# Kernel optimization log

Hardware: AMD Instinct MI355X
Metric: run time of the kernel (lower is better)

The kernel has to match this reference:

```python
import math
import jax, jax.numpy as jnp
import numpy as np

B, T, D = 2048, 50, 256
NEG = -100000.0

def setup_inputs() -> dict:
    key = jax.random.key(0)
    ks = jax.random.split(key, 9)
    return {
        "x": jax.random.normal(ks[0], (B, T, D), dtype=jnp.float32),
        "mask": jax.random.randint(ks[1], (B, T, 1), 0, 2, dtype=jnp.int32),
        "time_decay": jax.random.uniform(ks[2], (B, T, 1), dtype=jnp.float32),
        "Wq": jax.random.normal(ks[3], (D, D), dtype=jnp.float32) * (1.0 / math.sqrt(D)),
        "bq": jax.random.normal(ks[4], (D,), dtype=jnp.float32) * 0.01,
        "Wk": jax.random.normal(ks[5], (D, D), dtype=jnp.float32) * (1.0 / math.sqrt(D)),
        "bk": jax.random.normal(ks[6], (D,), dtype=jnp.float32) * 0.01,
        "Wv": jax.random.normal(ks[7], (D, D), dtype=jnp.float32) * (1.0 / math.sqrt(D)),
        "bv": jax.random.normal(ks[8], (D,), dtype=jnp.float32) * 0.01,
    }

def reference(x, mask, time_decay, Wq, bq, Wk, bk, Wv, bv):
    # PositionalEncoding.forward: elementwise multiply by time-decay (broadcast over d_model)
    x = x * time_decay  # [B,T,D]
    q = jnp.einsum('btd,ed->bte', x, Wq) + bq
    k = jnp.einsum('btd,ed->bte', x, Wk) + bk
    v = jnp.einsum('btd,ed->bte', x, Wv) + bv
    # unusual Q/K-side masking (masked_fill before the matmul)
    keep = mask != 0  # [B,T,1]
    q = jnp.where(keep, q, NEG)
    k = jnp.where(keep, k, NEG)
    score = jnp.einsum('btd,bsd->bts', q, k) / math.sqrt(D)  # [B,T,T]
    score = jax.nn.softmax(score, axis=-1)
    # dropout is identity in eval mode
    out = jnp.einsum('bts,bsd->btd', score, v)  # [B,T,D]
    return out[:, -1, :]  # [B,D]
```

## Files before the change

### kernel.cpp

```cpp
#include <hip/hip_runtime.h>


namespace {
constexpr int kB = 2048;
constexpr int kT = 50;
constexpr int kD = 256;
constexpr int kG = 4;
constexpr int kThr = 256;
constexpr double kNeg = -100000.0;
}

__global__ __launch_bounds__(kThr) void attn_fused(
    const float* __restrict__ x, const int* __restrict__ mask,
    const float* __restrict__ td, const float* __restrict__ Wq,
    const float* __restrict__ bq, const float* __restrict__ Wk,
    const float* __restrict__ bk, const float* __restrict__ Wv,
    const float* __restrict__ bv, float* __restrict__ out) {
  __shared__ __align__(16) float xs49[kG][kD];
  __shared__ __align__(16) float qf[kG][kD];
  __shared__ __align__(16) float ub[kG][kD];
  __shared__ __align__(16) float yb[kG][kD];
  __shared__ __align__(16) float cb[kD];
  __shared__ float tdb[kG * kT];
  __shared__ int mb[kG * kT];
  __shared__ double Sqb[kG], Qbkb[kG], sbkb;

  const int t = threadIdx.x;
  const int wave = t >> 6;
  const int lane = t & 63;
  const int b0 = blockIdx.x * kG;

  if (t < kG * kT) {
    tdb[t] = td[b0 * kT + t];
    mb[t] = mask[b0 * kT + t];
  }
  {
    const int g = t >> 6;
    const int c4 = t & 63;
    const float tv = td[(b0 + g) * kT + (kT - 1)];
    float4 xv =
        ((const float4*)(x + ((size_t)(b0 + g) * kT + kT - 1) * kD))[c4];
    xv.x *= tv; xv.y *= tv; xv.z *= tv; xv.w *= tv;
    ((float4*)(&xs49[g][0]))[c4] = xv;
  }
  __syncthreads();

  {
    const int e = t;
    float acc[kG] = {0.f, 0.f, 0.f, 0.f};
    const float4* wr = (const float4*)(Wq + (size_t)e * kD);
    for (int i = 0; i < kD / 4; ++i) {
      const float4 w = wr[i];
#pragma unroll
      for (int j = 0; j < kG; ++j) {
        const float4 a = ((const float4*)(&xs49[j][0]))[i];
        acc[j] += w.x * a.x + w.y * a.y + w.z * a.z + w.w * a.w;
      }
    }
    const float be = bq[e];
#pragma unroll
    for (int j = 0; j < kG; ++j) qf[j][e] = acc[j] + be;
  }
  __syncthreads();

  {
    const int g = wave;
    double s = 0.0, s2 = 0.0, s3 = 0.0;
#pragma unroll
    for (int i = 0; i < 4; ++i) {
      const int e = lane + 64 * i;
      const double q = (double)qf[g][e];
      const double bke = (double)bk[e];
      s += q;
      s2 += q * bke;
      s3 += bke;
    }
#pragma unroll
    for (int off = 32; off; off >>= 1) {
      s += __shfl_xor(s, off);
      s2 += __shfl_xor(s2, off);
      s3 += __shfl_xor(s3, off);
    }
    if (lane == 0) {
      Sqb[g] = s;
      Qbkb[g] = s2;
      if (g == 0) sbkb = s3;
    }
  }

  {
    const int d = t;
    float uacc[kG] = {0.f, 0.f, 0.f, 0.f};
    double cacc = 0.0;
    for (int e4 = 0; e4 < kD / 4; ++e4) {
      const float w0 = Wk[(size_t)(4 * e4 + 0) * kD + d];
      const float w1 = Wk[(size_t)(4 * e4 + 1) * kD + d];
      const float w2 = Wk[(size_t)(4 * e4 + 2) * kD + d];
      const float w3 = Wk[(size_t)(4 * e4 + 3) * kD + d];
#pragma unroll
      for (int j = 0; j < kG; ++j) {
        const float4 q4 = ((const float4*)(&qf[j][0]))[e4];
        uacc[j] += w0 * q4.x + w1 * q4.y + w2 * q4.z + w3 * q4.w;
      }
      cacc += (double)w0 + (double)w1 + (double)w2 + (double)w3;
    }
#pragma unroll
    for (int j = 0; j < kG; ++j) ub[j][d] = uacc[j];
    cb[d] = (float)cacc;
  }
  __syncthreads();

  {
    const int g = wave;
    const int b = b0 + g;
    const float4* xrow = (const float4*)(x + (size_t)b * kT * kD);
    const float4 u4 = ((const float4*)(&ub[g][0]))[lane];
    const float4 c4 = ((const float4*)(&cb[0]))[lane];
    const int mqg = mb[g * kT + (kT - 1)];
    float4 v4;
    v4.x = mqg ? u4.x : c4.x;
    v4.y = mqg ? u4.y : c4.y;
    v4.z = mqg ? u4.z : c4.z;
    v4.w = mqg ? u4.w : c4.w;
    const double Cm = kNeg * Sqb[g] * 0.0625;
    const double Cbb = 256.0 * 1.0e10 * 0.0625;
    const double Qbk = Qbkb[g];
    const double sbk = sbkb;

    double m = -1.0e300;
    float l = 0.f;
    float4 y = {0.f, 0.f, 0.f, 0.f};

    float4 n0 = xrow[0 * 64 + lane];
    float4 n1 = xrow[1 * 64 + lane];
    for (int s = 0; s < kT; s += 2) {
      const float4 r0 = n0, r1 = n1;
      if (s + 2 < kT) n0 = xrow[(s + 2) * 64 + lane];
      if (s + 3 < kT) n1 = xrow[(s + 3) * 64 + lane];
      const float tv0 = tdb[g * kT + s];
      const float tv1 = tdb[g * kT + s + 1];
      float4 a0, a1;
      a0.x = r0.x * tv0; a0.y = r0.y * tv0;
      a0.z = r0.z * tv0; a0.w = r0.w * tv0;
      a1.x = r1.x * tv1; a1.y = r1.y * tv1;
      a1.z = r1.z * tv1; a1.w = r1.w * tv1;
      float p0 = a0.x * v4.x + a0.y * v4.y + a0.z * v4.z + a0.w * v4.w;
      float p1 = a1.x * v4.x + a1.y * v4.y + a1.z * v4.z + a1.w * v4.w;
#pragma unroll
      for (int off = 32; off; off >>= 1) {
        p0 += __shfl_xor(p0, off);
        p1 += __shfl_xor(p1, off);
      }
      const int ms0 = mb[g * kT + s];
      const int ms1 = mb[g * kT + s + 1];
      double sc0, sc1;
      if (mqg) {
        sc0 = ms0 ? ((double)p0 + Qbk) * 0.0625 : Cm;
        sc1 = ms1 ? ((double)p1 + Qbk) * 0.0625 : Cm;
      } else {
        sc0 = ms0 ? kNeg * ((double)p0 + sbk) * 0.0625 : Cbb;
        sc1 = ms1 ? kNeg * ((double)p1 + sbk) * 0.0625 : Cbb;
      }
      double mnew = m;
      if (sc0 > mnew) mnew = sc0;
      if (sc1 > mnew) mnew = sc1;
      const float al = expf((float)(m - mnew));
      const float e0 = expf((float)(sc0 - mnew));
      const float e1 = expf((float)(sc1 - mnew));
      m = mnew;
      l = l * al + e0 + e1;
      y.x = y.x * al + e0 * a0.x + e1 * a1.x;
      y.y = y.y * al + e0 * a0.y + e1 * a1.y;
      y.z = y.z * al + e0 * a0.z + e1 * a1.z;
      y.w = y.w * al + e0 * a0.w + e1 * a1.w;
    }
    const float inv = 1.0f / l;
    y.x *= inv; y.y *= inv; y.z *= inv; y.w *= inv;
    ((float4*)(&yb[g][0]))[lane] = y;
  }
  __syncthreads();

  {
    const int e = t;
    float acc[kG] = {0.f, 0.f, 0.f, 0.f};
    const float4* wr = (const float4*)(Wv + (size_t)e * kD);
    for (int i = 0; i < kD / 4; ++i) {
      const float4 w = wr[i];
#pragma unroll
      for (int j = 0; j < kG; ++j) {
        const float4 yv = ((const float4*)(&yb[j][0]))[i];
        acc[j] += w.x * yv.x + w.y * yv.y + w.z * yv.z + w.w * yv.w;
      }
    }
    const float be = bv[e];
#pragma unroll
    for (int j = 0; j < kG; ++j)
      out[(size_t)(b0 + j) * kD + e] = acc[j] + be;
  }
}

extern "C" void kernel_launch(void* const* d_in, const int* in_sizes, int n_in,
                              void* d_out, int out_size, void* d_ws,
                              size_t ws_size, hipStream_t stream) {
  const float* x = (const float*)d_in[0];
  const int* mask = (const int*)d_in[1];
  const float* td = (const float*)d_in[2];
  const float* Wq = (const float*)d_in[3];
  const float* bq = (const float*)d_in[4];
  const float* Wk = (const float*)d_in[5];
  const float* bk = (const float*)d_in[6];
  const float* Wv = (const float*)d_in[7];
  const float* bv = (const float*)d_in[8];
  float* out = (float*)d_out;
  (void)d_ws; (void)ws_size; (void)in_sizes; (void)n_in; (void)out_size;

  hipLaunchKernelGGL(attn_fused, dim3(kB / kG), dim3(kThr), 0, stream, x, mask,
                     td, Wq, bq, Wk, bk, Wv, bv, out);
}
```

Measured before the change: 220.9 us.

## Precompute fused Wq·Wk product and transposed Wv in a prologue kernel

Adds a small precompute kernel that forms the Wq^T·Wk product, the bias-derived vectors and scalar constants, and a transposed copy of Wv in workspace. The main kernel then needs one 256x256 matvec per batch row instead of two (Q projection and then K-side), and reads weights coalesced for both matvecs. The batch group per block grows from 4 to 8 to amortize weight reads, and the online-softmax loop is unrolled by 4 with clamped prefetch. It adds an extra kernel launch and changes float rounding order, since the product is formed in fp32 ahead of time.

```diff
diff --git a/kernel.cpp b/kernel.cpp
--- a/kernel.cpp
+++ b/kernel.cpp
@@ -5,127 +5,198 @@
 constexpr int kB = 2048;
 constexpr int kT = 50;
 constexpr int kD = 256;
-constexpr int kG = 4;
+constexpr int kG = 8;
 constexpr int kThr = 256;
 constexpr double kNeg = -100000.0;
+constexpr int oM2 = 0;
+constexpr int oWvT = 65536;
+constexpr int oV0 = 131072;
+constexpr int oC = 131328;
+constexpr int oW1 = 131584;
+constexpr int oW2 = 131840;
+constexpr int oDbl = 132096;
 }
 
-__global__ __launch_bounds__(kThr) void attn_fused(
+__global__ __launch_bounds__(kThr) void precomp(
+    const float* __restrict__ Wq, const float* __restrict__ bq,
+    const float* __restrict__ Wk, const float* __restrict__ bk,
+    const float* __restrict__ Wv, float* __restrict__ ws) {
+  float* M2 = ws + oM2;
+  float* WvT = ws + oWvT;
+  double* dconst = (double*)(ws + oDbl);
+  const int t = threadIdx.x;
+  const int blk = blockIdx.x;
+  __shared__ float tile[64][65];
+  __shared__ double red[3][4];
+
+  if (blk < 64) {
+    const int a0 = blk * 4;
+    float acc0 = 0.f, acc1 = 0.f, acc2 = 0.f, acc3 = 0.f;
+    for (int e = 0; e < kD; e += 4) {
+#pragma unroll
+      for (int i = 0; i < 4; ++i) {
+        const float wk = Wk[(size_t)(e + i) * kD + t];
+        const float4 wq = *(const float4*)(Wq + (size_t)(e + i) * kD + a0);
+        acc0 += wq.x * wk;
+        acc1 += wq.y * wk;
+        acc2 += wq.z * wk;
+        acc3 += wq.w * wk;
+      }
+    }
+    M2[(size_t)(a0 + 0) * kD + t] = acc0;
+    M2[(size_t)(a0 + 1) * kD + t] = acc1;
+    M2[(size_t)(a0 + 2) * kD + t] = acc2;
+    M2[(size_t)(a0 + 3) * kD + t] = acc3;
+  } else if (blk < 68) {
+    const float* W = (blk < 66) ? Wk : Wq;
+    const float* coef = (blk == 64) ? bq : (blk == 66) ? bk : nullptr;
+    double acc = 0.0;
+    for (int e = 0; e < kD; e += 4) {
+#pragma unroll
+      for (int i = 0; i < 4; ++i) {
+        const double w = (double)W[(size_t)(e + i) * kD + t];
+        acc += coef ? (double)coef[e + i] * w : w;
+      }
+    }
+    float* dst = (blk == 64)   ? ws + oV0
+                 : (blk == 65) ? ws + oC
+                 : (blk == 66) ? ws + oW1
+                               : ws + oW2;
+    dst[t] = (float)acc;
+    if (blk == 65) {
+      double p0 = (double)bk[t];
+      double p1 = (double)bq[t] * (double)bk[t];
+      double p2 = (double)bq[t];
+      const int lane = t & 63, wv = t >> 6;
+#pragma unroll
+      for (int off = 32; off; off >>= 1) {
+        p0 += __shfl_xor(p0, off);
+        p1 += __shfl_xor(p1, off);
+        p2 += __shfl_xor(p2, off);
+      }
+      if (lane == 0) {
+        red[0][wv] = p0;
+        red[1][wv] = p1;
+        red[2][wv] = p2;
+      }
+      __syncthreads();
+      if (t == 0) {
+        dconst[0] = red[0][0] + red[0][1] + red[0][2] + red[0][3];
+        dconst[1] = red[1][0] + red[1][1] + red[1][2] + red[1][3];
+        dconst[2] = red[2][0] + red[2][1] + red[2][2] + red[2][3];
+      }
+    }
+  } else {
+    const int tb = blk - 68;
+    const int tr = tb >> 2, tc = tb & 3;
+    const int j = t & 63;
+#pragma unroll 4
+    for (int p = 0; p < 16; ++p) {
+      const int i = p * 4 + (t >> 6);
+      tile[i][j] = Wv[(size_t)(tr * 64 + i) * kD + tc * 64 + j];
+    }
+    __syncthreads();
+#pragma unroll 4
+    for (int p = 0; p < 16; ++p) {
+      const int r = p * 4 + (t >> 6);
+      WvT[(size_t)(tc * 64 + r) * kD + tr * 64 + j] = tile[j][r];
+    }
+  }
+}
+
+__global__ __launch_bounds__(kThr) void attn_main(
     const float* __restrict__ x, const int* __restrict__ mask,
-    const float* __restrict__ td, const float* __restrict__ Wq,
-    const float* __restrict__ bq, const float* __restrict__ Wk,
-    const float* __restrict__ bk, const float* __restrict__ Wv,
-    const float* __restrict__ bv, float* __restrict__ out) {
-  __shared__ __align__(16) float xs49[kG][kD];
-  __shared__ __align__(16) float qf[kG][kD];
+    const float* __restrict__ td, const float* __restrict__ bv,
+    const float* __restrict__ ws, float* __restrict__ out) {
+  const float* M2 = ws + oM2;
+  const float* WvT = ws + oWvT;
+  const float* v0 = ws + oV0;
+  const float* cv = ws + oC;
+  const float* w1 = ws + oW1;
+  const float* w2 = ws + oW2;
+  const double* dconst = (const double*)(ws + oDbl);
+
+  __shared__ __align__(16) float xs[kG][kD];
   __shared__ __align__(16) float ub[kG][kD];
   __shared__ __align__(16) float yb[kG][kD];
-  __shared__ __align__(16) float cb[kD];
   __shared__ float tdb[kG * kT];
   __shared__ int mb[kG * kT];
-  __shared__ double Sqb[kG], Qbkb[kG], sbkb;
+  __shared__ double Sqb[kG], Qbkb[kG];
 
   const int t = threadIdx.x;
   const int wave = t >> 6;
   const int lane = t & 63;
   const int b0 = blockIdx.x * kG;
 
-  if (t < kG * kT) {
-    tdb[t] = td[b0 * kT + t];
-    mb[t] = mask[b0 * kT + t];
-  }
-  {
-    const int g = t >> 6;
-    const int c4 = t & 63;
+  for (int idx = t; idx < kG * kT; idx += kThr) {
+    tdb[idx] = td[b0 * kT + idx];
+    mb[idx] = mask[b0 * kT + idx];
+  }
+  for (int idx = t; idx < kG * 64; idx += kThr) {
+    const int g = idx >> 6, c4 = idx & 63;
     const float tv = td[(b0 + g) * kT + (kT - 1)];
     float4 xv =
         ((const float4*)(x + ((size_t)(b0 + g) * kT + kT - 1) * kD))[c4];
     xv.x *= tv; xv.y *= tv; xv.z *= tv; xv.w *= tv;
-    ((float4*)(&xs49[g][0]))[c4] = xv;
+    ((float4*)(&xs[g][0]))[c4] = xv;
   }
   __syncthreads();
 
+#pragma unroll
+  for (int gb = 0; gb < 2; ++gb) {
+    const int g = wave * 2 + gb;
+    const float4 xv = ((const float4*)(&xs[g][0]))[lane];
+    const float4 a1 = ((const float4*)w1)[lane];
+    const float4 a2 = ((const float4*)w2)[lane];
+    double s1 = (double)xv.x * a1.x + (double)xv.y * a1.y +
+                (double)xv.z * a1.z + (double)xv.w * a1.w;
+    double s2 = (double)xv.x * a2.x + (double)xv.y * a2.y +
+                (double)xv.z * a2.z + (double)xv.w * a2.w;
+#pragma unroll
+    for (int off = 32; off; off >>= 1) {
+      s1 += __shfl_xor(s1, off);
+      s2 += __shfl_xor(s2, off);
+    }
+    if (lane == 0) {
+      Qbkb[g] = s1 + dconst[1];
+      Sqb[g] = s2 + dconst[2];
+    }
+  }
+
   {
-    const int e = t;
-    float acc[kG] = {0.f, 0.f, 0.f, 0.f};
-    const float4* wr = (const float4*)(Wq + (size_t)e * kD);
-    for (int i = 0; i < kD / 4; ++i) {
-      const float4 w = wr[i];
+    float acc[kG];
+    const float v0t = v0[t];
+#pragma unroll
+    for (int j = 0; j < kG; ++j) acc[j] = v0t;
+    for (int dd = 0; dd < kD; dd += 4) {
+      const float m0 = M2[(size_t)(dd + 0) * kD + t];
+      const float m1 = M2[(size_t)(dd + 1) * kD + t];
+      const float m2 = M2[(size_t)(dd + 2) * kD + t];
+      const float m3 = M2[(size_t)(dd + 3) * kD + t];
 #pragma unroll
       for (int j = 0; j < kG; ++j) {
-        const float4 a = ((const float4*)(&xs49[j][0]))[i];
-        acc[j] += w.x * a.x + w.y * a.y + w.z * a.z + w.w * a.w;
-      }
-    }
-    const float be = bq[e];
-#pragma unroll
-    for (int j = 0; j < kG; ++j) qf[j][e] = acc[j] + be;
+        const float4 xj = *(const float4*)(&xs[j][dd]);
+        acc[j] += xj.x * m0 + xj.y * m1 + xj.z * m2 + xj.w * m3;
+      }
+    }
+#pragma unroll
+    for (int j = 0; j < kG; ++j) ub[j][t] = acc[j];
   }
   __syncthreads();
 
-  {
-    const int g = wave;
-    double s = 0.0, s2 = 0.0, s3 = 0.0;
-#pragma unroll
-    for (int i = 0; i < 4; ++i) {
-      const int e = lane + 64 * i;
-      const double q = (double)qf[g][e];
-      const double bke = (double)bk[e];
-      s += q;
-      s2 += q * bke;
-      s3 += bke;
-    }
-#pragma unroll
-    for (int off = 32; off; off >>= 1) {
-      s += __shfl_xor(s, off);
-      s2 += __shfl_xor(s2, off);
-      s3 += __shfl_xor(s3, off);
-    }
-    if (lane == 0) {
-      Sqb[g] = s;
-      Qbkb[g] = s2;
-      if (g == 0) sbkb = s3;
-    }
-  }
-
-  {
-    const int d = t;
-    float uacc[kG] = {0.f, 0.f, 0.f, 0.f};
-    double cacc = 0.0;
-    for (int e4 = 0; e4 < kD / 4; ++e4) {
-      const float w0 = Wk[(size_t)(4 * e4 + 0) * kD + d];
-      const float w1 = Wk[(size_t)(4 * e4 + 1) * kD + d];
-      const float w2 = Wk[(size_t)(4 * e4 + 2) * kD + d];
-      const float w3 = Wk[(size_t)(4 * e4 + 3) * kD + d];
-#pragma unroll
-      for (int j = 0; j < kG; ++j) {
-        const float4 q4 = ((const float4*)(&qf[j][0]))[e4];
-        uacc[j] += w0 * q4.x + w1 * q4.y + w2 * q4.z + w3 * q4.w;
-      }
-      cacc += (double)w0 + (double)w1 + (double)w2 + (double)w3;
-    }
-#pragma unroll
-    for (int j = 0; j < kG; ++j) ub[j][d] = uacc[j];
-    cb[d] = (float)cacc;
-  }
-  __syncthreads();
-
-  {
-    const int g = wave;
+  const double sbkd = dconst[0];
+  const double Cbb = 256.0 * 1.0e10 * 0.0625;
+  for (int gb = 0; gb < 2; ++gb) {
+    const int g = wave * 2 + gb;
     const int b = b0 + g;
+    const int base = g * kT;
     const float4* xrow = (const float4*)(x + (size_t)b * kT * kD);
     const float4 u4 = ((const float4*)(&ub[g][0]))[lane];
-    const float4 c4 = ((const float4*)(&cb[0]))[lane];
-    const int mqg = mb[g * kT + (kT - 1)];
-    float4 v4;
-    v4.x = mqg ? u4.x : c4.x;
-    v4.y = mqg ? u4.y : c4.y;
-    v4.z = mqg ? u4.z : c4.z;
-    v4.w = mqg ? u4.w : c4.w;
+    const float4 c4 = ((const float4*)cv)[lane];
+    const int mqg = mb[base + (kT - 1)];
+    const float4 v4 = mqg ? u4 : c4;
     const double Cm = kNeg * Sqb[g] * 0.0625;
-    const double Cbb = 256.0 * 1.0e10 * 0.0625;
     const double Qbk = Qbkb[g];
-    const double sbk = sbkb;
 
     double m = -1.0e300;
     float l = 0.f;
@@ -133,46 +204,80 @@
 
     float4 n0 = xrow[0 * 64 + lane];
     float4 n1 = xrow[1 * 64 + lane];
-    for (int s = 0; s < kT; s += 2) {
-      const float4 r0 = n0, r1 = n1;
-      if (s + 2 < kT) n0 = xrow[(s + 2) * 64 + lane];
-      if (s + 3 < kT) n1 = xrow[(s + 3) * 64 + lane];
-      const float tv0 = tdb[g * kT + s];
-      const float tv1 = tdb[g * kT + s + 1];
-      float4 a0, a1;
-      a0.x = r0.x * tv0; a0.y = r0.y * tv0;
-      a0.z = r0.z * tv0; a0.w = r0.w * tv0;
-      a1.x = r1.x * tv1; a1.y = r1.y * tv1;
-      a1.z = r1.z * tv1; a1.w = r1.w * tv1;
+    float4 n2 = xrow[2 * 64 + lane];
+    float4 n3 = xrow[3 * 64 + lane];
+    for (int s = 0; s < 52; s += 4) {
+      const float4 r0 = n0, r1 = n1, r2 = n2, r3 = n3;
+      {
+        const int p0 = (s + 4 < kT) ? s + 4 : kT - 1;
+        const int p1 = (s + 5 < kT) ? s + 5 : kT - 1;
+        const int p2 = (s + 6 < kT) ? s + 6 : kT - 1;
+        const int p3 = (s + 7 < kT) ? s + 7 : kT - 1;
+        n0 = xrow[p0 * 64 + lane];
+        n1 = xrow[p1 * 64 + lane];
+        n2 = xrow[p2 * 64 + lane];
+        n3 = xrow[p3 * 64 + lane];
+      }
+      const int s0i = s, s1i = s + 1, s2i = s + 2, s3i = s + 3;
+      const int c0 = (s0i < kT) ? s0i : kT - 1;
+      const int c1 = (s1i < kT) ? s1i : kT - 1;
+      const int c2 = (s2i < kT) ? s2i : kT - 1;
+      const int c3 = (s3i < kT) ? s3i : kT - 1;
+      const float tv0 = tdb[base + c0];
+      const float tv1 = tdb[base + c1];
+      const float tv2 = tdb[base + c2];
+      const float tv3 = tdb[base + c3];
+      float4 a0, a1, a2, a3;
+      a0.x = r0.x * tv0; a0.y = r0.y * tv0; a0.z = r0.z * tv0; a0.w = r0.w * tv0;
+      a1.x = r1.x * tv1; a1.y = r1.y * tv1; a1.z = r1.z * tv1; a1.w = r1.w * tv1;
+      a2.x = r2.x * tv2; a2.y = r2.y * tv2; a2.z = r2.z * tv2; a2.w = r2.w * tv2;
+      a3.x = r3.x * tv3; a3.y = r3.y * tv3; a3.z = r3.z * tv3; a3.w = r3.w * tv3;
       float p0 = a0.x * v4.x + a0.y * v4.y + a0.z * v4.z + a0.w * v4.w;
       float p1 = a1.x * v4.x + a1.y * v4.y + a1.z * v4.z + a1.w * v4.w;
+      float p2 = a2.x * v4.x + a2.y * v4.y + a2.z * v4.z + a2.w * v4.w;
+      float p3 = a3.x * v4.x + a3.y * v4.y + a3.z * v4.z + a3.w * v4.w;
 #pragma unroll
       for (int off = 32; off; off >>= 1) {
         p0 += __shfl_xor(p0, off);
         p1 += __shfl_xor(p1, off);
-      }
-      const int ms0 = mb[g * kT + s];
-      const int ms1 = mb[g * kT + s + 1];
-      double sc0, sc1;
+        p2 += __shfl_xor(p2, off);
+        p3 += __shfl_xor(p3, off);
+      }
+      const int ms0 = mb[base + c0];
+      const int ms1 = mb[base + c1];
+      const int ms2 = mb[base + c2];
+      const int ms3 = mb[base + c3];
+      double sc0, sc1, sc2, sc3;
       if (mqg) {
         sc0 = ms0 ? ((double)p0 + Qbk) * 0.0625 : Cm;
         sc1 = ms1 ? ((double)p1 + Qbk) * 0.0625 : Cm;
+        sc2 = ms2 ? ((double)p2 + Qbk) * 0.0625 : Cm;
+        sc3 = ms3 ? ((double)p3 + Qbk) * 0.0625 : Cm;
       } else {
-        sc0 = ms0 ? kNeg * ((double)p0 + sbk) * 0.0625 : Cbb;
-        sc1 = ms1 ? kNeg * ((double)p1 + sbk) * 0.0625 : Cbb;
-      }
+        sc0 = ms0 ? kNeg * ((double)p0 + sbkd) * 0.0625 : Cbb;
+        sc1 = ms1 ? kNeg * ((double)p1 + sbkd) * 0.0625 : Cbb;
+        sc2 = ms2 ? kNeg * ((double)p2 + sbkd) * 0.0625 : Cbb;
+        sc3 = ms3 ? kNeg * ((double)p3 + sbkd) * 0.0625 : Cbb;
+      }
+      if (s1i >= kT) sc1 = -1.0e300;
+      if (s2i >= kT) sc2 = -1.0e300;
+      if (s3i >= kT) sc3 = -1.0e300;
       double mnew = m;
       if (sc0 > mnew) mnew = sc0;
       if (sc1 > mnew) mnew = sc1;
+      if (sc2 > mnew) mnew = sc2;
+      if (sc3 > mnew) mnew = sc3;
       const float al = expf((float)(m - mnew));
       const float e0 = expf((float)(sc0 - mnew));
       const float e1 = expf((float)(sc1 - mnew));
+      const float e2 = expf((float)(sc2 - mnew));
+      const float e3 = expf((float)(sc3 - mnew));
       m = mnew;
-      l = l * al + e0 + e1;
-      y.x = y.x * al + e0 * a0.x + e1 * a1.x;
-      y.y = y.y * al + e0 * a0.y + e1 * a1.y;
-      y.z = y.z * al + e0 * a0.z + e1 * a1.z;
-      y.w = y.w * al + e0 * a0.w + e1 * a1.w;
+      l = l * al + e0 + e1 + e2 + e3;
+      y.x = y.x * al + e0 * a0.x + e1 * a1.x + e2 * a2.x + e3 * a3.x;
+      y.y = y.y * al + e0 * a0.y + e1 * a1.y + e2 * a2.y + e3 * a3.y;
+      y.z = y.z * al + e0 * a0.z + e1 * a1.z + e2 * a2.z + e3 * a3.z;
+      y.w = y.w * al + e0 * a0.w + e1 * a1.w + e2 * a2.w + e3 * a3.w;
     }
     const float inv = 1.0f / l;
     y.x *= inv; y.y *= inv; y.z *= inv; y.w *= inv;
@@ -181,21 +286,23 @@
   __syncthreads();
 
   {
-    const int e = t;
-    float acc[kG] = {0.f, 0.f, 0.f, 0.f};
-    const float4* wr = (const float4*)(Wv + (size_t)e * kD);
-    for (int i = 0; i < kD / 4; ++i) {
-      const float4 w = wr[i];
+    float acc[kG];
+    const float bvt = bv[t];
+#pragma unroll
+    for (int j = 0; j < kG; ++j) acc[j] = bvt;
+    for (int dd = 0; dd < kD; dd += 4) {
+      const float m0 = WvT[(size_t)(dd + 0) * kD + t];
+      const float m1 = WvT[(size_t)(dd + 1) * kD + t];
+      const float m2 = WvT[(size_t)(dd + 2) * kD + t];
+      const float m3 = WvT[(size_t)(dd + 3) * kD + t];
 #pragma unroll
       for (int j = 0; j < kG; ++j) {
-        const float4 yv = ((const float4*)(&yb[j][0]))[i];
-        acc[j] += w.x * yv.x + w.y * yv.y + w.z * yv.z + w.w * yv.w;
-      }
-    }
-    const float be = bv[e];
-#pragma unroll
-    for (int j = 0; j < kG; ++j)
-      out[(size_t)(b0 + j) * kD + e] = acc[j] + be;
+        const float4 yj = *(const float4*)(&yb[j][dd]);
+        acc[j] += yj.x * m0 + yj.y * m1 + yj.z * m2 + yj.w * m3;
+      }
+    }
+#pragma unroll
+    for (int j = 0; j < kG; ++j) out[(size_t)(b0 + j) * kD + t] = acc[j];
   }
 }
 
@@ -211,9 +318,12 @@
   const float* bk = (const float*)d_in[6];
   const float* Wv = (const float*)d_in[7];
   const float* bv = (const float*)d_in[8];
+  float* ws = (float*)d_ws;
   float* out = (float*)d_out;
-  (void)d_ws; (void)ws_size; (void)in_sizes; (void)n_in; (void)out_size;
-
-  hipLaunchKernelGGL(attn_fused, dim3(kB / kG), dim3(kThr), 0, stream, x, mask,
-                     td, Wq, bq, Wk, bk, Wv, bv, out);
+  (void)in_sizes; (void)n_in; (void)out_size; (void)ws_size;
+
+  hipLaunchKernelGGL(precomp, dim3(84), dim3(kThr), 0, stream, Wq, bq, Wk, bk,
+                     Wv, ws);
+  hipLaunchKernelGGL(attn_main, dim3(kB / kG), dim3(kThr), 0, stream, x, mask,
+                     td, bv, (const float*)ws, out);
 }
```

Result: slower. 266.8 us (+20.8%).
